# Performance work log

Hardware: AMD Instinct MI355X
Metric: run time of the kernel (lower is better)

The kernel has to match this reference:

```python
import jax, jax.numpy as jnp
import numpy as np

KERNEL_LAM = 0.003


def setup_inputs() -> dict:
    key = jax.random.key(0)
    ks = jax.random.split(key, 5)
    B, H, L, Lk = 2, 2048, 4096, 128
    u = jax.random.normal(ks[0], (B, H, L), dtype=jnp.float32)
    kernel = jax.random.normal(ks[1], (1, H, Lk), dtype=jnp.float32) * 0.002
    D = jax.random.normal(ks[2], (1, H), dtype=jnp.float32)
    W_out = jax.random.normal(ks[3], (2 * H, H), dtype=jnp.float32) / np.sqrt(H)
    b_out = jnp.zeros((2 * H,), dtype=jnp.float32)
    return {"u": u, "kernel": kernel, "D": D, "W_out": W_out, "b_out": b_out}


def reference(u, kernel, D, W_out, b_out):
    # u: [B, H, L]; kernel: [C=1, H, Lk]; D: [C, H]; W_out: [2H, H]; b_out: [2H]
    B, H, L = u.shape
    n = 2 * L
    # soft-threshold kernel
    k = jax.nn.relu(jnp.abs(kernel) - KERNEL_LAM) * jnp.sign(kernel)
    k_f = jnp.fft.rfft(k, n=n)            # [C, H, L+1] complex
    u_f = jnp.fft.rfft(u, n=n)            # [B, H, L+1] complex
    y_f = jnp.einsum('bhl,chl->bchl', u_f, k_f)
    y = jnp.fft.irfft(y_f, n=n)[..., :L]  # [B, C, H, L]
    y = y + jnp.einsum('bhl,ch->bchl', u, D)
    y = y.reshape(B, -1, L)               # [B, C*H, L]
    y = jax.nn.gelu(y, approximate=False)
    # output_linear: 1x1 conv H -> 2H, then GLU over channel dim
    y = jnp.einsum('oh,bhl->bol', W_out, y) + b_out[None, :, None]
    a, g = jnp.split(y, 2, axis=1)
    return a * jax.nn.sigmoid(g)          # [B, H, L]
```

## Files before the change

kernel.cpp:

```cpp
#include <hip/hip_runtime.h>
#include <stdint.h>

typedef short short8 __attribute__((ext_vector_type(8)));
typedef float f32x4 __attribute__((ext_vector_type(4)));

#define KLAM 0.003f

__device__ __forceinline__ uint16_t f2bf(float f) {
  union { float f; uint32_t u; } v; v.f = f;
  uint32_t r = v.u + 0x7fffu + ((v.u >> 16) & 1u);
  return (uint16_t)(r >> 16);
}
__device__ __forceinline__ uint32_t pack_lo(uint32_t a, uint32_t b) { return (a & 0xffffu) | (b << 16); }
__device__ __forceinline__ uint32_t pack_hi(uint32_t a, uint32_t b) { return (a >> 16) | (b & 0xffff0000u); }
__device__ __forceinline__ int swzB(int n) { return ((n & 7) ^ ((n >> 3) & 7)); }

typedef __attribute__((address_space(3))) uint32_t* lds_u32p;
typedef const __attribute__((address_space(1))) uint32_t* gbl_u32p;
__device__ __forceinline__ void gload16(const void* g, void* l) {
  __builtin_amdgcn_global_load_lds((gbl_u32p)g, (lds_u32p)l, 16, 0, 0);
}

__global__ __launch_bounds__(256) void cast_w_kernel(const float* __restrict__ W,
                                                     uint16_t* __restrict__ Wb) {
  int i = (blockIdx.x * 256 + threadIdx.x) * 8;
  float4 f0 = *(const float4*)(W + i);
  float4 f1 = *(const float4*)(W + i + 4);
  uint4 q;
  q.x = (uint32_t)f2bf(f0.x) | ((uint32_t)f2bf(f0.y) << 16);
  q.y = (uint32_t)f2bf(f0.z) | ((uint32_t)f2bf(f0.w) << 16);
  q.z = (uint32_t)f2bf(f1.x) | ((uint32_t)f2bf(f1.y) << 16);
  q.w = (uint32_t)f2bf(f1.z) | ((uint32_t)f2bf(f1.w) << 16);
  *(uint4*)(Wb + i) = q;
}

__global__ __launch_bounds__(256) void conv_gelu_kernel(const float* __restrict__ u,
                                                        const float* __restrict__ kern,
                                                        const float* __restrict__ D,
                                                        uint16_t* __restrict__ X) {
  __shared__ __align__(16) float su[4096];
  __shared__ __align__(16) uint16_t ubf[4256];
  __shared__ __align__(16) uint16_t kR[176];
  __shared__ __align__(16) uint16_t stg[4][256];

  int tid = threadIdx.x;
  int bh = blockIdx.x;
  int h = bh & 2047;
  int b = bh >> 11;
  int lane = tid & 63;
  int wv = tid >> 6;
  int ln15 = lane & 15;
  int g = lane >> 4;

  const float4* u4 = (const float4*)(u + (size_t)bh * 4096);
#pragma unroll
  for (int i = 0; i < 4; ++i) {
    float4 v = u4[i * 256 + tid];
    ((float4*)su)[i * 256 + tid] = v;
    uint2 p;
    p.x = (uint32_t)f2bf(v.x) | ((uint32_t)f2bf(v.y) << 16);
    p.y = (uint32_t)f2bf(v.z) | ((uint32_t)f2bf(v.w) << 16);
    *(uint2*)(ubf + 160 + (i * 256 + tid) * 4) = p;
  }
  if (tid < 40) { uint2 z; z.x = 0; z.y = 0; *(uint2*)(ubf + tid * 4) = z; }
  if (tid < 176) {
    int i = 159 - tid;
    uint16_t r = 0;
    if (i >= 0 && i < 128) {
      float kv = kern[h * 128 + i];
      float a = fabsf(kv) - KLAM;
      float s = (a > 0.f) ? (kv > 0.f ? a : -a) : 0.f;
      r = f2bf(s);
    }
    kR[tid] = r;
  }
  __syncthreads();

  float Dh = D[h];

  short8 bfr[5];
#pragma unroll
  for (int q = 0; q < 5; ++q) {
    int z0 = 143 - 32 * q - ln15 + 8 * g;
    union { short8 v; uint16_t s[8]; } t;
#pragma unroll
    for (int e = 0; e < 8; ++e) t.s[e] = kR[z0 + e];
    bfr[q] = t.v;
  }

#pragma unroll
  for (int it = 0; it < 4; ++it) {
    int T0 = (wv * 4 + it) * 256;
    f32x4 acc = {0.f, 0.f, 0.f, 0.f};
#pragma unroll
    for (int q = 0; q < 5; ++q) {
      const short8 a = *(const short8*)(ubf + 160 + T0 + 16 * ln15 - 16 - 32 * q + 8 * g);
      acc = __builtin_amdgcn_mfma_f32_16x16x32_bf16(a, bfr[q], acc, 0, 0, 0);
    }
#pragma unroll
    for (int r = 0; r < 4; ++r) {
      int m = 4 * g + r;
      int t = T0 + 16 * m + ln15;
      float y = acc[r] + Dh * su[t];
      float ge = 0.5f * y * (1.f + erff(y * 0.70710678118654752f));
      stg[wv][16 * m + ln15] = f2bf(ge);
    }
    uint2 v = *(uint2*)(&stg[wv][lane * 4]);
    *(uint2*)(X + (size_t)h * 8192 + (size_t)b * 4096 + T0 + lane * 4) = v;
  }
}

__global__ __launch_bounds__(256) void transpose_kernel(const uint16_t* __restrict__ X,
                                                        uint16_t* __restrict__ XT) {
  __shared__ uint16_t t[64][66];
  int tid = threadIdx.x;
  int bn = blockIdx.x & 127;
  int bk = blockIdx.x >> 7;
  int n0 = bn << 6, k0 = bk << 6;
  int cr = tid >> 3;
  int cc = (tid & 7) * 8;
#pragma unroll
  for (int p = 0; p < 2; ++p) {
    int kr = p * 32 + cr;
    uint4 v = *(const uint4*)(X + (size_t)(k0 + kr) * 8192 + n0 + cc);
    const uint16_t* s = (const uint16_t*)&v;
#pragma unroll
    for (int e = 0; e < 8; ++e) t[cc + e][kr] = s[e];
  }
  __syncthreads();
#pragma unroll
  for (int p = 0; p < 2; ++p) {
    int nl = p * 32 + cr;
    uint16_t d[8];
#pragma unroll
    for (int e = 0; e < 8; ++e) d[e] = t[nl][cc + e];
    *(uint4*)(XT + (size_t)(n0 + nl) * 2048 + k0 + cc) = *(uint4*)d;
  }
}

__global__ __launch_bounds__(512, 2) void gemm_glu_v3(const uint16_t* __restrict__ Wb,
                                                      const uint16_t* __restrict__ XT,
                                                      const float* __restrict__ bout,
                                                      float* __restrict__ out) {
  __shared__ __align__(16) char lds[131072];

  int tid = threadIdx.x;
  int lane = tid & 63;
  int wv = tid >> 6;
  int wr = wv >> 2;
  int wc = wv & 3;
  int ln15 = lane & 15;
  int g16 = lane >> 4;

  int bid = blockIdx.x;
  int wg = (bid & 7) * 64 + (bid >> 3);
  int bm = wg >> 5, bn = wg & 31;
  int mo0 = bm * 128, n0 = bn * 256;

  int lr8 = lane >> 3;
  int sb = (((lane & 7) ^ lr8) << 4);
  const char* wbB = (const char*)Wb;
  const char* xtB = (const char*)XT;
  const char* srcAA = wbB + (size_t)(mo0 + wv * 16 + lr8) * 4096 + sb;
  const char* srcAG = wbB + (size_t)(2048 + mo0 + wv * 16 + lr8) * 4096 + sb;
  const char* srcBL = xtB + (size_t)(n0 + wv * 16 + lr8) * 4096 + sb;
  const char* srcBH = xtB + (size_t)(n0 + 128 + wv * 16 + lr8) * 4096 + sb;
  uint32_t ldW = wv * 2048;

  auto stageAA = [&](int buf, int t) {
    size_t ko = (size_t)t * 128;
    char* d = lds + buf * 32768 + ldW;
    gload16(srcAA + ko, d);
    gload16(srcAA + ko + 32768, d + 1024);
  };
  auto stageAG = [&](int buf, int t) {
    size_t ko = (size_t)t * 128;
    char* d = lds + buf * 32768 + 16384 + ldW;
    gload16(srcAG + ko, d);
    gload16(srcAG + ko + 32768, d + 1024);
  };
  auto stageBL = [&](int buf, int t) {
    size_t ko = (size_t)t * 128;
    char* d = lds + 65536 + buf * 32768 + ldW;
    gload16(srcBL + ko, d);
    gload16(srcBL + ko + 32768, d + 1024);
  };
  auto stageBH = [&](int buf, int t) {
    size_t ko = (size_t)t * 128;
    char* d = lds + 65536 + buf * 32768 + 16384 + ldW;
    gload16(srcBH + ko, d);
    gload16(srcBH + ko + 32768, d + 1024);
  };

  f32x4 zero = {0.f, 0.f, 0.f, 0.f};
  f32x4 acc_a[4][4], acc_g[4][4];
#pragma unroll
  for (int mi = 0; mi < 4; ++mi)
#pragma unroll
    for (int ni = 0; ni < 4; ++ni) { acc_a[mi][ni] = zero; acc_g[mi][ni] = zero; }

  stageAA(0, 0); stageBL(0, 0); stageAG(0, 0); stageBH(0, 0);
  stageAA(1, 1); stageBL(1, 1); stageAG(1, 1);
  asm volatile("s_waitcnt vmcnt(6)" ::: "memory");
  __builtin_amdgcn_s_barrier();

  short8 fa[4][2], fg[4][2], fb[4][2];

  for (int t = 0; t < 32; ++t) {
    int cur = t & 1;
    const char* A = lds + cur * 32768;
    const char* Bb = lds + 65536 + cur * 32768;

#pragma unroll
    for (int mi = 0; mi < 4; ++mi) {
      int ra = wr * 64 + mi * 16 + ln15;
      int sw = (ra & 7) << 4;
#pragma unroll
      for (int kk = 0; kk < 2; ++kk)
        fa[mi][kk] = *(const short8*)(A + ra * 128 + ((kk * 64 + g16 * 16) ^ sw));
    }
#pragma unroll
    for (int ni = 0; ni < 2; ++ni) {
      int n = wc * 64 + ni * 16 + ln15;
      int sw = (n & 7) << 4;
#pragma unroll
      for (int kk = 0; kk < 2; ++kk)
        fb[ni][kk] = *(const short8*)(Bb + n * 128 + ((kk * 64 + g16 * 16) ^ sw));
    }
    if (t < 31) stageBH(cur ^ 1, t + 1);
    __builtin_amdgcn_s_barrier();
    asm volatile("s_waitcnt lgkmcnt(0)" ::: "memory");
    __builtin_amdgcn_s_setprio(1);
#pragma unroll
    for (int mi = 0; mi < 4; ++mi)
#pragma unroll
      for (int ni = 0; ni < 2; ++ni)
#pragma unroll
        for (int kk = 0; kk < 2; ++kk)
          acc_a[mi][ni] = __builtin_amdgcn_mfma_f32_16x16x32_bf16(fa[mi][kk], fb[ni][kk], acc_a[mi][ni], 0, 0, 0);
    __builtin_amdgcn_s_setprio(0);
    __builtin_amdgcn_s_barrier();

#pragma unroll
    for (int ni = 2; ni < 4; ++ni) {
      int n = wc * 64 + ni * 16 + ln15;
      int sw = (n & 7) << 4;
#pragma unroll
      for (int kk = 0; kk < 2; ++kk)
        fb[ni][kk] = *(const short8*)(Bb + n * 128 + ((kk * 64 + g16 * 16) ^ sw));
    }
    if (t < 30) stageAA(cur, t + 2);
    __builtin_amdgcn_s_barrier();
    asm volatile("s_waitcnt lgkmcnt(0)" ::: "memory");
    __builtin_amdgcn_s_setprio(1);
#pragma unroll
    for (int mi = 0; mi < 4; ++mi)
#pragma unroll
      for (int ni = 2; ni < 4; ++ni)
#pragma unroll
        for (int kk = 0; kk < 2; ++kk)
          acc_a[mi][ni] = __builtin_amdgcn_mfma_f32_16x16x32_bf16(fa[mi][kk], fb[ni][kk], acc_a[mi][ni], 0, 0, 0);
    __builtin_amdgcn_s_setprio(0);
    __builtin_amdgcn_s_barrier();

#pragma unroll
    for (int mi = 0; mi < 4; ++mi) {
      int rg = 128 + wr * 64 + mi * 16 + ln15;
      int sw = (rg & 7) << 4;
#pragma unroll
      for (int kk = 0; kk < 2; ++kk)
        fg[mi][kk] = *(const short8*)(A + rg * 128 + ((kk * 64 + g16 * 16) ^ sw));
    }
    if (t < 30) stageBL(cur, t + 2);
    __builtin_amdgcn_s_barrier();
    asm volatile("s_waitcnt lgkmcnt(0)" ::: "memory");
    __builtin_amdgcn_s_setprio(1);
#pragma unroll
    for (int mi = 0; mi < 4; ++mi)
#pragma unroll
      for (int ni = 0; ni < 2; ++ni)
#pragma unroll
        for (int kk = 0; kk < 2; ++kk)
          acc_g[mi][ni] = __builtin_amdgcn_mfma_f32_16x16x32_bf16(fg[mi][kk], fb[ni][kk], acc_g[mi][ni], 0, 0, 0);
    __builtin_amdgcn_s_setprio(0);
    __builtin_amdgcn_s_barrier();

    if (t < 30) stageAG(cur, t + 2);
    if (t < 30) { asm volatile("s_waitcnt vmcnt(6)" ::: "memory"); }
    else        { asm volatile("s_waitcnt vmcnt(0)" ::: "memory"); }
    __builtin_amdgcn_s_barrier();
    __builtin_amdgcn_s_setprio(1);
#pragma unroll
    for (int mi = 0; mi < 4; ++mi)
#pragma unroll
      for (int ni = 2; ni < 4; ++ni)
#pragma unroll
        for (int kk = 0; kk < 2; ++kk)
          acc_g[mi][ni] = __builtin_amdgcn_mfma_f32_16x16x32_bf16(fg[mi][kk], fb[ni][kk], acc_g[mi][ni], 0, 0, 0);
    __builtin_amdgcn_s_setprio(0);
    __builtin_amdgcn_s_barrier();
  }

#pragma unroll
  for (int mi = 0; mi < 4; ++mi) {
    int ob = mo0 + wr * 64 + mi * 16 + g16 * 4;
    float4 ba4 = *(const float4*)(bout + ob);
    float4 bg4 = *(const float4*)(bout + ob + 2048);
    const float* bap = (const float*)&ba4;
    const float* bgp = (const float*)&bg4;
#pragma unroll
    for (int q = 0; q < 4; ++q) {
      int o = ob + q;
#pragma unroll
      for (int ni = 0; ni < 4; ++ni) {
        float av = acc_a[mi][ni][q] + bap[q];
        float gv = acc_g[mi][ni][q] + bgp[q];
        float res = av / (1.f + expf(-gv));
        int n = n0 + wc * 64 + ni * 16 + ln15;
        out[(size_t)(n >> 12) * 8388608 + (size_t)o * 4096 + (n & 4095)] = res;
      }
    }
  }
}

__global__ __launch_bounds__(256, 2) void gemm_glu_v1(const uint16_t* __restrict__ Wb,
                                                      const uint16_t* __restrict__ X,
                                                      const float* __restrict__ bout,
                                                      float* __restrict__ out) {
  __shared__ char lds[65536];

  int tid = threadIdx.x;
  int lane = tid & 63;
  int wv = tid >> 6;

  int bid = blockIdx.x;
  int wg = (bid & 7) * 256 + (bid >> 3);
  int bm = wg >> 6, bn = wg & 63;
  int m0 = bm * 64, n0 = bn * 128;

  int arb = tid >> 3;
  int ab = (tid & 7) * 16;
  const char* Aglob[4];
  uint32_t AwAddr[4];
#pragma unroll
  for (int i = 0; i < 4; ++i) {
    int r = i * 32 + arb;
    int o = (r < 64) ? (m0 + r) : (2048 + m0 + (r - 64));
    Aglob[i] = (const char*)Wb + (size_t)o * 4096 + ab;
    AwAddr[i] = (uint32_t)(r * 128 + (ab ^ ((r & 7) << 4)));
  }
  int n4 = (tid & 31) * 4;
  int kg = (tid >> 5) * 8;
  const char* Bglob = (const char*)X + ((size_t)kg * 8192 + (size_t)(n0 + n4)) * 2;
  uint32_t BwAddr[4];
#pragma unroll
  for (int no = 0; no < 4; ++no) {
    int n = n4 + no;
    BwAddr[no] = (uint32_t)(n * 128 + (((tid >> 5) * 16) ^ (swzB(n) << 4)));
  }

  f32x4 zero = {0.f, 0.f, 0.f, 0.f};
  f32x4 acc_a[2][4], acc_g[2][4];
#pragma unroll
  for (int mi = 0; mi < 2; ++mi)
#pragma unroll
    for (int ni = 0; ni < 4; ++ni) { acc_a[mi][ni] = zero; acc_g[mi][ni] = zero; }

  uint4 aR[4];
  uint2 bR[8];
  auto LOAD = [&](int t) {
    size_t koff = (size_t)t * 128;
#pragma unroll
    for (int i = 0; i < 4; ++i) aR[i] = *(const uint4*)(Aglob[i] + koff);
    size_t bko = (size_t)t * 64 * 16384;
#pragma unroll
    for (int i = 0; i < 8; ++i) bR[i] = *(const uint2*)(Bglob + bko + (size_t)i * 16384);
  };
  auto WRITE = [&](int buf) {
    char* A = lds + buf * 16384;
#pragma unroll
    for (int i = 0; i < 4; ++i) *(uint4*)(A + AwAddr[i]) = aR[i];
    char* Bb = lds + 32768 + buf * 16384;
    {
      uint4 q; q.x = pack_lo(bR[0].x, bR[1].x); q.y = pack_lo(bR[2].x, bR[3].x);
      q.z = pack_lo(bR[4].x, bR[5].x); q.w = pack_lo(bR[6].x, bR[7].x);
      *(uint4*)(Bb + BwAddr[0]) = q;
    }
    {
      uint4 q; q.x = pack_hi(bR[0].x, bR[1].x); q.y = pack_hi(bR[2].x, bR[3].x);
      q.z = pack_hi(bR[4].x, bR[5].x); q.w = pack_hi(bR[6].x, bR[7].x);
      *(uint4*)(Bb + BwAddr[1]) = q;
    }
    {
      uint4 q; q.x = pack_lo(bR[0].y, bR[1].y); q.y = pack_lo(bR[2].y, bR[3].y);
      q.z = pack_lo(bR[4].y, bR[5].y); q.w = pack_lo(bR[6].y, bR[7].y);
      *(uint4*)(Bb + BwAddr[2]) = q;
    }
    {
      uint4 q; q.x = pack_hi(bR[0].y, bR[1].y); q.y = pack_hi(bR[2].y, bR[3].y);
      q.z = pack_hi(bR[4].y, bR[5].y); q.w = pack_hi(bR[6].y, bR[7].y);
      *(uint4*)(Bb + BwAddr[3]) = q;
    }
  };

  LOAD(0);
  WRITE(0);
  __syncthreads();

  for (int t = 0; t < 32; ++t) {
    int cur = t & 1;
    if (t < 31) LOAD(t + 1);

    const char* A = lds + cur * 16384;
    const char* Bb = lds + 32768 + cur * 16384;
#pragma unroll
    for (int kk = 0; kk < 2; ++kk) {
      int kbyte = kk * 64 + ((lane >> 4) << 4);
      short8 fa[2], fg[2], fb[4];
#pragma unroll
      for (int mi = 0; mi < 2; ++mi) {
        int ra = (wv >> 1) * 32 + mi * 16 + (lane & 15);
        fa[mi] = *(const short8*)(A + ra * 128 + (kbyte ^ ((ra & 7) << 4)));
        int rg = 64 + ra;
        fg[mi] = *(const short8*)(A + rg * 128 + (kbyte ^ ((rg & 7) << 4)));
      }
#pragma unroll
      for (int ni = 0; ni < 4; ++ni) {
        int n = (wv & 1) * 64 + ni * 16 + (lane & 15);
        fb[ni] = *(const short8*)(Bb + n * 128 + (kbyte ^ (swzB(n) << 4)));
      }
#pragma unroll
      for (int mi = 0; mi < 2; ++mi)
#pragma unroll
        for (int ni = 0; ni < 4; ++ni) {
          acc_a[mi][ni] = __builtin_amdgcn_mfma_f32_16x16x32_bf16(fa[mi], fb[ni], acc_a[mi][ni], 0, 0, 0);
          acc_g[mi][ni] = __builtin_amdgcn_mfma_f32_16x16x32_bf16(fg[mi], fb[ni], acc_g[mi][ni], 0, 0, 0);
        }
    }

    if (t < 31) WRITE(cur ^ 1);
    __syncthreads();
  }

  int colb = n0 + (wv & 1) * 64;
#pragma unroll
  for (int mi = 0; mi < 2; ++mi) {
    int ob = m0 + (wv >> 1) * 32 + mi * 16 + ((lane >> 4) << 2);
#pragma unroll
    for (int q = 0; q < 4; ++q) {
      int o = ob + q;
      float ba = bout[o];
      float bg = bout[o + 2048];
#pragma unroll
      for (int ni = 0; ni < 4; ++ni) {
        float av = acc_a[mi][ni][q] + ba;
        float gv = acc_g[mi][ni][q] + bg;
        float res = av / (1.f + expf(-gv));
        int n = colb + ni * 16 + (lane & 15);
        out[(size_t)(n >> 12) * 8388608 + (size_t)o * 4096 + (n & 4095)] = res;
      }
    }
  }
}

extern "C" void kernel_launch(void* const* d_in, const int* in_sizes, int n_in,
                              void* d_out, int out_size, void* d_ws, size_t ws_size,
                              hipStream_t stream) {
  const float* u    = (const float*)d_in[0];
  const float* kern = (const float*)d_in[1];
  const float* D    = (const float*)d_in[2];
  const float* W    = (const float*)d_in[3];
  const float* bo   = (const float*)d_in[4];
  float* out = (float*)d_out;

  uint16_t* Wb = (uint16_t*)d_ws;
  uint16_t* X  = (uint16_t*)((char*)d_ws + (size_t)16 * 1024 * 1024);
  uint16_t* XT = (uint16_t*)((char*)d_ws + (size_t)48 * 1024 * 1024);

  hipLaunchKernelGGL(cast_w_kernel,    dim3(4096), dim3(256), 0, stream, W, Wb);
  hipLaunchKernelGGL(conv_gelu_kernel, dim3(4096), dim3(256), 0, stream, u, kern, D, X);
  if (ws_size >= (size_t)80 * 1024 * 1024) {
    hipLaunchKernelGGL(transpose_kernel, dim3(4096), dim3(256), 0, stream, X, XT);
    hipLaunchKernelGGL(gemm_glu_v3,      dim3(512),  dim3(512), 0, stream, Wb, XT, bo, out);
  } else {
    hipLaunchKernelGGL(gemm_glu_v1,      dim3(2048), dim3(256), 0, stream, Wb, X, bo, out);
  }
}
```

Before: 184.2 us.

## Prefetch next A fragments during last MFMA phase and remap tiles per XCD

Moves the LDS reads of the next k-tile's A fragments into the final MFMA phase of the current tile, so they overlap gate MFMAs instead of stalling at the start of the next iteration. The loop is manually unrolled by two with compile-time buffer indices. Block-to-tile mapping now gives each XCD a contiguous group of N columns with M varying, aiming for better L2 reuse of the B operand. The change adds register pressure from overlapping fragment lifetimes under the 2-waves launch bound.

Result: slower. 193.0 us (+4.8%).

```diff
diff --git a/kernel.cpp b/kernel.cpp
--- a/kernel.cpp
+++ b/kernel.cpp
@@ -138,7 +138,7 @@
   }
 }
 
-__global__ __launch_bounds__(512, 2) void gemm_glu_v3(const uint16_t* __restrict__ Wb,
+__global__ __launch_bounds__(512, 2) void gemm_glu_v4(const uint16_t* __restrict__ Wb,
                                                       const uint16_t* __restrict__ XT,
                                                       const float* __restrict__ bout,
                                                       float* __restrict__ out) {
@@ -153,8 +153,9 @@
   int g16 = lane >> 4;
 
   int bid = blockIdx.x;
-  int wg = (bid & 7) * 64 + (bid >> 3);
-  int bm = wg >> 5, bn = wg & 31;
+  int xcd = bid & 7, idx = bid >> 3;
+  int bn = xcd * 4 + (idx & 3);
+  int bm = idx >> 2;
   int mo0 = bm * 128, n0 = bn * 256;
 
   int lr8 = lane >> 3;
@@ -199,106 +200,106 @@
 #pragma unroll
     for (int ni = 0; ni < 4; ++ni) { acc_a[mi][ni] = zero; acc_g[mi][ni] = zero; }
 
+  short8 fa[4][2], fg[4][2], fb[4][2];
+
+  auto READ_FA = [&](const char* A) {
+#pragma unroll
+    for (int mi = 0; mi < 4; ++mi) {
+      int ra = wr * 64 + mi * 16 + ln15;
+      int sw = (ra & 7) << 4;
+      fa[mi][0] = *(const short8*)(A + ra * 128 + ((g16 * 16) ^ sw));
+      fa[mi][1] = *(const short8*)(A + ra * 128 + ((64 + g16 * 16) ^ sw));
+    }
+  };
+  auto READ_FG = [&](const char* A) {
+#pragma unroll
+    for (int mi = 0; mi < 4; ++mi) {
+      int rg = 128 + wr * 64 + mi * 16 + ln15;
+      int sw = (rg & 7) << 4;
+      fg[mi][0] = *(const short8*)(A + rg * 128 + ((g16 * 16) ^ sw));
+      fg[mi][1] = *(const short8*)(A + rg * 128 + ((64 + g16 * 16) ^ sw));
+    }
+  };
+  auto READ_FB2 = [&](const char* Bb, int nbase) {
+#pragma unroll
+    for (int ni = 0; ni < 2; ++ni) {
+      int n = wc * 64 + (nbase + ni) * 16 + ln15;
+      int sw = (n & 7) << 4;
+      fb[nbase + ni][0] = *(const short8*)(Bb + n * 128 + ((g16 * 16) ^ sw));
+      fb[nbase + ni][1] = *(const short8*)(Bb + n * 128 + ((64 + g16 * 16) ^ sw));
+    }
+  };
+
+  auto MFMA_A = [&](int nbase) {
+    __builtin_amdgcn_s_setprio(1);
+#pragma unroll
+    for (int mi = 0; mi < 4; ++mi)
+#pragma unroll
+      for (int ni = nbase; ni < nbase + 2; ++ni)
+#pragma unroll
+        for (int kk = 0; kk < 2; ++kk)
+          acc_a[mi][ni] = __builtin_amdgcn_mfma_f32_16x16x32_bf16(fa[mi][kk], fb[ni][kk], acc_a[mi][ni], 0, 0, 0);
+    __builtin_amdgcn_s_setprio(0);
+  };
+  auto MFMA_G = [&](int nbase) {
+    __builtin_amdgcn_s_setprio(1);
+#pragma unroll
+    for (int mi = 0; mi < 4; ++mi)
+#pragma unroll
+      for (int ni = nbase; ni < nbase + 2; ++ni)
+#pragma unroll
+        for (int kk = 0; kk < 2; ++kk)
+          acc_g[mi][ni] = __builtin_amdgcn_mfma_f32_16x16x32_bf16(fg[mi][kk], fb[ni][kk], acc_g[mi][ni], 0, 0, 0);
+    __builtin_amdgcn_s_setprio(0);
+  };
+
   stageAA(0, 0); stageBL(0, 0); stageAG(0, 0); stageBH(0, 0);
   stageAA(1, 1); stageBL(1, 1); stageAG(1, 1);
   asm volatile("s_waitcnt vmcnt(6)" ::: "memory");
   __builtin_amdgcn_s_barrier();
-
-  short8 fa[4][2], fg[4][2], fb[4][2];
-
-  for (int t = 0; t < 32; ++t) {
-    int cur = t & 1;
+  READ_FA(lds + 0);
+
+  auto KTILE = [&](int t, int cur) {
     const char* A = lds + cur * 32768;
     const char* Bb = lds + 65536 + cur * 32768;
-
-#pragma unroll
-    for (int mi = 0; mi < 4; ++mi) {
-      int ra = wr * 64 + mi * 16 + ln15;
-      int sw = (ra & 7) << 4;
-#pragma unroll
-      for (int kk = 0; kk < 2; ++kk)
-        fa[mi][kk] = *(const short8*)(A + ra * 128 + ((kk * 64 + g16 * 16) ^ sw));
-    }
-#pragma unroll
-    for (int ni = 0; ni < 2; ++ni) {
-      int n = wc * 64 + ni * 16 + ln15;
-      int sw = (n & 7) << 4;
-#pragma unroll
-      for (int kk = 0; kk < 2; ++kk)
-        fb[ni][kk] = *(const short8*)(Bb + n * 128 + ((kk * 64 + g16 * 16) ^ sw));
-    }
+    const char* Anext = lds + (cur ^ 1) * 32768;
+
+    READ_FB2(Bb, 0);
     if (t < 31) stageBH(cur ^ 1, t + 1);
     __builtin_amdgcn_s_barrier();
     asm volatile("s_waitcnt lgkmcnt(0)" ::: "memory");
-    __builtin_amdgcn_s_setprio(1);
-#pragma unroll
-    for (int mi = 0; mi < 4; ++mi)
-#pragma unroll
-      for (int ni = 0; ni < 2; ++ni)
-#pragma unroll
-        for (int kk = 0; kk < 2; ++kk)
-          acc_a[mi][ni] = __builtin_amdgcn_mfma_f32_16x16x32_bf16(fa[mi][kk], fb[ni][kk], acc_a[mi][ni], 0, 0, 0);
-    __builtin_amdgcn_s_setprio(0);
-    __builtin_amdgcn_s_barrier();
-
-#pragma unroll
-    for (int ni = 2; ni < 4; ++ni) {
-      int n = wc * 64 + ni * 16 + ln15;
-      int sw = (n & 7) << 4;
-#pragma unroll
-      for (int kk = 0; kk < 2; ++kk)
-        fb[ni][kk] = *(const short8*)(Bb + n * 128 + ((kk * 64 + g16 * 16) ^ sw));
-    }
+    MFMA_A(0);
+    __builtin_amdgcn_s_barrier();
+
+    READ_FB2(Bb, 2);
     if (t < 30) stageAA(cur, t + 2);
     __builtin_amdgcn_s_barrier();
     asm volatile("s_waitcnt lgkmcnt(0)" ::: "memory");
-    __builtin_amdgcn_s_setprio(1);
-#pragma unroll
-    for (int mi = 0; mi < 4; ++mi)
-#pragma unroll
-      for (int ni = 2; ni < 4; ++ni)
-#pragma unroll
-        for (int kk = 0; kk < 2; ++kk)
-          acc_a[mi][ni] = __builtin_amdgcn_mfma_f32_16x16x32_bf16(fa[mi][kk], fb[ni][kk], acc_a[mi][ni], 0, 0, 0);
-    __builtin_amdgcn_s_setprio(0);
-    __builtin_amdgcn_s_barrier();
-
-#pragma unroll
-    for (int mi = 0; mi < 4; ++mi) {
-      int rg = 128 + wr * 64 + mi * 16 + ln15;
-      int sw = (rg & 7) << 4;
-#pragma unroll
-      for (int kk = 0; kk < 2; ++kk)
-        fg[mi][kk] = *(const short8*)(A + rg * 128 + ((kk * 64 + g16 * 16) ^ sw));
-    }
+    MFMA_A(2);
+    __builtin_amdgcn_s_barrier();
+
+    READ_FG(A);
     if (t < 30) stageBL(cur, t + 2);
     __builtin_amdgcn_s_barrier();
     asm volatile("s_waitcnt lgkmcnt(0)" ::: "memory");
-    __builtin_amdgcn_s_setprio(1);
-#pragma unroll
-    for (int mi = 0; mi < 4; ++mi)
-#pragma unroll
-      for (int ni = 0; ni < 2; ++ni)
-#pragma unroll
-        for (int kk = 0; kk < 2; ++kk)
-          acc_g[mi][ni] = __builtin_amdgcn_mfma_f32_16x16x32_bf16(fg[mi][kk], fb[ni][kk], acc_g[mi][ni], 0, 0, 0);
-    __builtin_amdgcn_s_setprio(0);
-    __builtin_amdgcn_s_barrier();
-
-    if (t < 30) stageAG(cur, t + 2);
-    if (t < 30) { asm volatile("s_waitcnt vmcnt(6)" ::: "memory"); }
-    else        { asm volatile("s_waitcnt vmcnt(0)" ::: "memory"); }
-    __builtin_amdgcn_s_barrier();
-    __builtin_amdgcn_s_setprio(1);
-#pragma unroll
-    for (int mi = 0; mi < 4; ++mi)
-#pragma unroll
-      for (int ni = 2; ni < 4; ++ni)
-#pragma unroll
-        for (int kk = 0; kk < 2; ++kk)
-          acc_g[mi][ni] = __builtin_amdgcn_mfma_f32_16x16x32_bf16(fg[mi][kk], fb[ni][kk], acc_g[mi][ni], 0, 0, 0);
-    __builtin_amdgcn_s_setprio(0);
-    __builtin_amdgcn_s_barrier();
+    MFMA_G(0);
+    __builtin_amdgcn_s_barrier();
+
+    if (t < 30) {
+      stageAG(cur, t + 2);
+      asm volatile("s_waitcnt vmcnt(6)" ::: "memory");
+    } else {
+      asm volatile("s_waitcnt vmcnt(0)" ::: "memory");
+    }
+    __builtin_amdgcn_s_barrier();
+    if (t < 31) READ_FA(Anext);
+    MFMA_G(2);
+    __builtin_amdgcn_s_barrier();
+  };
+
+  for (int tt = 0; tt < 16; ++tt) {
+    KTILE(2 * tt, 0);
+    KTILE(2 * tt + 1, 1);
   }
 
 #pragma unroll
@@ -481,7 +482,7 @@
   hipLaunchKernelGGL(conv_gelu_kernel, dim3(4096), dim3(256), 0, stream, u, kern, D, X);
   if (ws_size >= (size_t)80 * 1024 * 1024) {
     hipLaunchKernelGGL(transpose_kernel, dim3(4096), dim3(256), 0, stream, X, XT);
-    hipLaunchKernelGGL(gemm_glu_v3,      dim3(512),  dim3(512), 0, stream, Wb, XT, bo, out);
+    hipLaunchKernelGGL(gemm_glu_v4,      dim3(512),  dim3(512), 0, stream, Wb, XT, bo, out);
   } else {
     hipLaunchKernelGGL(gemm_glu_v1,      dim3(2048), dim3(256), 0, stream, Wb, X, bo, out);
   }
```

## Remap GEMM tiles per XCD and precompute LDS offsets with 2x-unrolled k-loop

Applied to the files above, without the earlier changes.

Changes the block-to-tile mapping so each XCD handles 4 N-column tiles across all M-row tiles, instead of 2 M-rows across all 32 N-columns. This shrinks the per-XCD working set and should improve L2 reuse of the transposed activations and weights. It also replaces per-iteration LDS address arithmetic with precomputed offsets and incrementing global pointers. The k-loop is unrolled by two so the double-buffer index becomes a compile-time constant. An extra partial lgkmcnt wait is added before the first barrier.

Result: no change. 181.7 us (-1.3%).

```diff
diff --git a/kernel.cpp b/kernel.cpp
--- a/kernel.cpp
+++ b/kernel.cpp
@@ -138,7 +138,7 @@
   }
 }
 
-__global__ __launch_bounds__(512, 2) void gemm_glu_v3(const uint16_t* __restrict__ Wb,
+__global__ __launch_bounds__(512, 2) void gemm_glu_v7(const uint16_t* __restrict__ Wb,
                                                       const uint16_t* __restrict__ XT,
                                                       const float* __restrict__ bout,
                                                       float* __restrict__ out) {
@@ -153,44 +153,41 @@
   int g16 = lane >> 4;
 
   int bid = blockIdx.x;
-  int wg = (bid & 7) * 64 + (bid >> 3);
-  int bm = wg >> 5, bn = wg & 31;
+  int xcd = bid & 7, idx = bid >> 3;
+  int bn = xcd * 4 + (idx & 3);
+  int bm = idx >> 2;
   int mo0 = bm * 128, n0 = bn * 256;
 
   int lr8 = lane >> 3;
   int sb = (((lane & 7) ^ lr8) << 4);
-  const char* wbB = (const char*)Wb;
-  const char* xtB = (const char*)XT;
-  const char* srcAA = wbB + (size_t)(mo0 + wv * 16 + lr8) * 4096 + sb;
-  const char* srcAG = wbB + (size_t)(2048 + mo0 + wv * 16 + lr8) * 4096 + sb;
-  const char* srcBL = xtB + (size_t)(n0 + wv * 16 + lr8) * 4096 + sb;
-  const char* srcBH = xtB + (size_t)(n0 + 128 + wv * 16 + lr8) * 4096 + sb;
+  const char* pAA = (const char*)Wb + (size_t)(mo0 + wv * 16 + lr8) * 4096 + sb;
+  const char* pAG = (const char*)Wb + (size_t)(2048 + mo0 + wv * 16 + lr8) * 4096 + sb;
+  const char* pBL = (const char*)XT + (size_t)(n0 + wv * 16 + lr8) * 4096 + sb;
+  const char* pBH = (const char*)XT + (size_t)(n0 + 128 + wv * 16 + lr8) * 4096 + sb;
   uint32_t ldW = wv * 2048;
 
-  auto stageAA = [&](int buf, int t) {
-    size_t ko = (size_t)t * 128;
+  auto stAA = [&](int buf, const char* p) {
     char* d = lds + buf * 32768 + ldW;
-    gload16(srcAA + ko, d);
-    gload16(srcAA + ko + 32768, d + 1024);
-  };
-  auto stageAG = [&](int buf, int t) {
-    size_t ko = (size_t)t * 128;
+    gload16(p, d); gload16(p + 32768, d + 1024);
+  };
+  auto stAG = [&](int buf, const char* p) {
     char* d = lds + buf * 32768 + 16384 + ldW;
-    gload16(srcAG + ko, d);
-    gload16(srcAG + ko + 32768, d + 1024);
-  };
-  auto stageBL = [&](int buf, int t) {
-    size_t ko = (size_t)t * 128;
+    gload16(p, d); gload16(p + 32768, d + 1024);
+  };
+  auto stBL = [&](int buf, const char* p) {
     char* d = lds + 65536 + buf * 32768 + ldW;
-    gload16(srcBL + ko, d);
-    gload16(srcBL + ko + 32768, d + 1024);
-  };
-  auto stageBH = [&](int buf, int t) {
-    size_t ko = (size_t)t * 128;
+    gload16(p, d); gload16(p + 32768, d + 1024);
+  };
+  auto stBH = [&](int buf, const char* p) {
     char* d = lds + 65536 + buf * 32768 + 16384 + ldW;
-    gload16(srcBH + ko, d);
-    gload16(srcBH + ko + 32768, d + 1024);
-  };
+    gload16(p, d); gload16(p + 32768, d + 1024);
+  };
+
+  int sw = (ln15 & 7) << 4;
+  uint32_t aoff0 = (uint32_t)((wr * 64 + ln15) * 128 + ((g16 * 16) ^ sw));
+  uint32_t aoff1 = (uint32_t)((wr * 64 + ln15) * 128 + ((64 + g16 * 16) ^ sw));
+  uint32_t boff0 = (uint32_t)(65536 + (wc * 64 + ln15) * 128 + ((g16 * 16) ^ sw));
+  uint32_t boff1 = (uint32_t)(65536 + (wc * 64 + ln15) * 128 + ((64 + g16 * 16) ^ sw));
 
   f32x4 zero = {0.f, 0.f, 0.f, 0.f};
   f32x4 acc_a[4][4], acc_g[4][4];
@@ -199,35 +196,27 @@
 #pragma unroll
     for (int ni = 0; ni < 4; ++ni) { acc_a[mi][ni] = zero; acc_g[mi][ni] = zero; }
 
-  stageAA(0, 0); stageBL(0, 0); stageAG(0, 0); stageBH(0, 0);
-  stageAA(1, 1); stageBL(1, 1); stageAG(1, 1);
+  short8 fa[4][2], fg[4][2], fb[4][2];
+
+  stAA(0, pAA); stBL(0, pBL); stAG(0, pAG); stBH(0, pBH);
+  stAA(1, pAA + 128); stBL(1, pBL + 128); stAG(1, pAG + 128);
+  pAA += 256; pBL += 256; pAG += 256; pBH += 128;
   asm volatile("s_waitcnt vmcnt(6)" ::: "memory");
   __builtin_amdgcn_s_barrier();
 
-  short8 fa[4][2], fg[4][2], fb[4][2];
-
-  for (int t = 0; t < 32; ++t) {
-    int cur = t & 1;
-    const char* A = lds + cur * 32768;
-    const char* Bb = lds + 65536 + cur * 32768;
-
+  auto KTILE = [&](int t, int cur) {
 #pragma unroll
     for (int mi = 0; mi < 4; ++mi) {
-      int ra = wr * 64 + mi * 16 + ln15;
-      int sw = (ra & 7) << 4;
-#pragma unroll
-      for (int kk = 0; kk < 2; ++kk)
-        fa[mi][kk] = *(const short8*)(A + ra * 128 + ((kk * 64 + g16 * 16) ^ sw));
+      fa[mi][0] = *(const short8*)(lds + cur * 32768 + mi * 2048 + aoff0);
+      fa[mi][1] = *(const short8*)(lds + cur * 32768 + mi * 2048 + aoff1);
     }
 #pragma unroll
     for (int ni = 0; ni < 2; ++ni) {
-      int n = wc * 64 + ni * 16 + ln15;
-      int sw = (n & 7) << 4;
-#pragma unroll
-      for (int kk = 0; kk < 2; ++kk)
-        fb[ni][kk] = *(const short8*)(Bb + n * 128 + ((kk * 64 + g16 * 16) ^ sw));
-    }
-    if (t < 31) stageBH(cur ^ 1, t + 1);
+      fb[ni][0] = *(const short8*)(lds + cur * 32768 + ni * 2048 + boff0);
+      fb[ni][1] = *(const short8*)(lds + cur * 32768 + ni * 2048 + boff1);
+    }
+    if (t < 31) stBH(cur ^ 1, pBH);
+    asm volatile("s_waitcnt lgkmcnt(8)" ::: "memory");
     __builtin_amdgcn_s_barrier();
     asm volatile("s_waitcnt lgkmcnt(0)" ::: "memory");
     __builtin_amdgcn_s_setprio(1);
@@ -243,13 +232,10 @@
 
 #pragma unroll
     for (int ni = 2; ni < 4; ++ni) {
-      int n = wc * 64 + ni * 16 + ln15;
-      int sw = (n & 7) << 4;
-#pragma unroll
-      for (int kk = 0; kk < 2; ++kk)
-        fb[ni][kk] = *(const short8*)(Bb + n * 128 + ((kk * 64 + g16 * 16) ^ sw));
-    }
-    if (t < 30) stageAA(cur, t + 2);
+      fb[ni][0] = *(const short8*)(lds + cur * 32768 + ni * 2048 + boff0);
+      fb[ni][1] = *(const short8*)(lds + cur * 32768 + ni * 2048 + boff1);
+    }
+    if (t < 30) stAA(cur, pAA);
     __builtin_amdgcn_s_barrier();
     asm volatile("s_waitcnt lgkmcnt(0)" ::: "memory");
     __builtin_amdgcn_s_setprio(1);
@@ -265,13 +251,10 @@
 
 #pragma unroll
     for (int mi = 0; mi < 4; ++mi) {
-      int rg = 128 + wr * 64 + mi * 16 + ln15;
-      int sw = (rg & 7) << 4;
-#pragma unroll
-      for (int kk = 0; kk < 2; ++kk)
-        fg[mi][kk] = *(const short8*)(A + rg * 128 + ((kk * 64 + g16 * 16) ^ sw));
-    }
-    if (t < 30) stageBL(cur, t + 2);
+      fg[mi][0] = *(const short8*)(lds + cur * 32768 + 16384 + mi * 2048 + aoff0);
+      fg[mi][1] = *(const short8*)(lds + cur * 32768 + 16384 + mi * 2048 + aoff1);
+    }
+    if (t < 30) stBL(cur, pBL);
     __builtin_amdgcn_s_barrier();
     asm volatile("s_waitcnt lgkmcnt(0)" ::: "memory");
     __builtin_amdgcn_s_setprio(1);
@@ -285,9 +268,12 @@
     __builtin_amdgcn_s_setprio(0);
     __builtin_amdgcn_s_barrier();
 
-    if (t < 30) stageAG(cur, t + 2);
-    if (t < 30) { asm volatile("s_waitcnt vmcnt(6)" ::: "memory"); }
-    else        { asm volatile("s_waitcnt vmcnt(0)" ::: "memory"); }
+    if (t < 30) {
+      stAG(cur, pAG);
+      asm volatile("s_waitcnt vmcnt(6)" ::: "memory");
+    } else {
+      asm volatile("s_waitcnt vmcnt(0)" ::: "memory");
+    }
     __builtin_amdgcn_s_barrier();
     __builtin_amdgcn_s_setprio(1);
 #pragma unroll
@@ -299,6 +285,13 @@
           acc_g[mi][ni] = __builtin_amdgcn_mfma_f32_16x16x32_bf16(fg[mi][kk], fb[ni][kk], acc_g[mi][ni], 0, 0, 0);
     __builtin_amdgcn_s_setprio(0);
     __builtin_amdgcn_s_barrier();
+
+    pAA += 128; pBL += 128; pAG += 128; pBH += 128;
+  };
+
+  for (int tt = 0; tt < 16; ++tt) {
+    KTILE(2 * tt, 0);
+    KTILE(2 * tt + 1, 1);
   }
 
 #pragma unroll
@@ -481,7 +474,7 @@
   hipLaunchKernelGGL(conv_gelu_kernel, dim3(4096), dim3(256), 0, stream, u, kern, D, X);
   if (ws_size >= (size_t)80 * 1024 * 1024) {
     hipLaunchKernelGGL(transpose_kernel, dim3(4096), dim3(256), 0, stream, X, XT);
-    hipLaunchKernelGGL(gemm_glu_v3,      dim3(512),  dim3(512), 0, stream, Wb, XT, bo, out);
+    hipLaunchKernelGGL(gemm_glu_v7,      dim3(512),  dim3(512), 0, stream, Wb, XT, bo, out);
   } else {
     hipLaunchKernelGGL(gemm_glu_v1,      dim3(2048), dim3(256), 0, stream, Wb, X, bo, out);
   }
```
